# Kernel tuning notes

Measured on AMD Instinct MI355X. Metric: run time of the kernel, lower is better.

The kernel has to match this reference:

```python
import jax, jax.numpy as jnp
import numpy as np

N_NODES = 100000
N_EDGES = 1600000
IN_DIM, HID_DIM, OUT_DIM = 128, 256, 512
BN_EPS = 1e-5


def setup_inputs() -> dict:
    key = jax.random.key(0)
    ks = jax.random.split(key, 10)
    x = jax.random.normal(ks[0], (N_NODES, IN_DIM), dtype=jnp.float32)
    edge_index = jax.random.randint(ks[1], (2, N_EDGES), 0, N_NODES, dtype=jnp.int64)
    def lin(k, o, i):
        return jax.random.normal(k, (o, i), dtype=jnp.float32) * (1.0 / np.sqrt(i))
    return {
        "x": x,
        "edge_index": edge_index,
        # SAGEConv 1: in_dim -> hidden_dim (lin_l has bias, lin_r has none)
        "W1l": lin(ks[2], HID_DIM, IN_DIM),
        "b1": jnp.zeros((HID_DIM,), dtype=jnp.float32),
        "W1r": lin(ks[3], HID_DIM, IN_DIM),
        # BatchNorm1d(hidden_dim)
        "gamma": jnp.ones((HID_DIM,), dtype=jnp.float32),
        "beta": jnp.zeros((HID_DIM,), dtype=jnp.float32),
        # SAGEConv 2: hidden_dim -> gnn_out_dim
        "W2l": lin(ks[4], OUT_DIM, HID_DIM),
        "b2": jnp.zeros((OUT_DIM,), dtype=jnp.float32),
        "W2r": lin(ks[5], OUT_DIM, HID_DIM),
    }


def _sage_max(h, src, dst, Wl, b, Wr, n_nodes):
    # gather source features, max-aggregate onto destination nodes
    agg = jax.ops.segment_max(h[src], dst, num_segments=n_nodes)  # [N, D]
    agg = jnp.where(jnp.isneginf(agg), 0.0, agg)  # PyG fills empty segments with 0
    return agg @ Wl.T + b + h @ Wr.T


def reference(x, edge_index, W1l, b1, W1r, gamma, beta, W2l, b2, W2r):
    src, dst = edge_index[0], edge_index[1]
    n = x.shape[0]
    # layer 1: SAGEConv(in_dim, hidden_dim, aggr='max')
    h = _sage_max(x, src, dst, W1l, b1, W1r, n)
    # BatchNorm1d (batch statistics), Dropout is identity in eval; no activation in 'sage' branch
    mean = jnp.mean(h, axis=0)
    var = jnp.var(h, axis=0)
    h = gamma * (h - mean) * jax.lax.rsqrt(var + BN_EPS) + beta
    # layer 2: SAGEConv(hidden_dim, gnn_out_dim, aggr='max')
    out = _sage_max(h, src, dst, W2l, b2, W2r, n)
    return out
```

## Files before the change

kernel.cpp:

```cpp
#include <hip/hip_runtime.h>
#include <hip/hip_bf16.h>
#include <stdint.h>

#define N_NODES 100000
#define N_EDGES 1600000
#define IN_DIM 128
#define HID_DIM 256
#define OUT_DIM 512
#define NBUK 391
#define BCAP 8192
#define EPB 4096

typedef __attribute__((ext_vector_type(4))) float f32x4;
typedef __attribute__((ext_vector_type(8))) short bf16x8;

__device__ __forceinline__ float bf16lo(uint32_t u){ uint32_t b = u << 16; return __builtin_bit_cast(float, b); }
__device__ __forceinline__ float bf16hi(uint32_t u){ uint32_t b = u & 0xffff0000u; return __builtin_bit_cast(float, b); }
__device__ __forceinline__ uint16_t f32_to_bf16(float f){
  uint32_t u = __builtin_bit_cast(uint32_t, f);
  uint32_t r = (u + 0x7fffu + ((u >> 16) & 1u)) >> 16;
  return (uint16_t)r;
}
__device__ __forceinline__ uint32_t pack_bf16_exact(float lo, float hi){
  return (__builtin_bit_cast(uint32_t, hi) & 0xffff0000u) | (__builtin_bit_cast(uint32_t, lo) >> 16);
}
__device__ __forceinline__ uint32_t pack_bf16_rne(float lo, float hi){
  return (uint32_t)f32_to_bf16(lo) | ((uint32_t)f32_to_bf16(hi) << 16);
}
__device__ __forceinline__ void gl2lds16(const void* g, void* l){
  __builtin_amdgcn_global_load_lds(
      (const __attribute__((address_space(1))) uint32_t*)g,
      (__attribute__((address_space(3))) uint32_t*)l, 16, 0, 0);
}

__global__ void k_convx(const float* __restrict__ x, uint16_t* __restrict__ A1,
                        int* __restrict__ gcur, float* __restrict__ sum,
                        float* __restrict__ sumsq){
  if (blockIdx.x == 12500){
    const int t = threadIdx.x;
    for (int i = t; i < NBUK; i += 256) gcur[i] = i << 13;
    sum[t] = 0.f; sumsq[t] = 0.f;
    return;
  }
  const int idx = blockIdx.x * 256 + threadIdx.x;
  const int n = idx >> 5, q = idx & 31;
  const float4 v = *(const float4*)(x + (long)n * 128 + q * 4);
  ushort4 o;
  o.x = f32_to_bf16(v.x); o.y = f32_to_bf16(v.y);
  o.z = f32_to_bf16(v.z); o.w = f32_to_bf16(v.w);
  *(ushort4*)(A1 + (long)n * 256 + 128 + q * 4) = o;
}

__global__ void k_bucket(const int* __restrict__ src, const int* __restrict__ dst,
                         int* __restrict__ gcur, int* __restrict__ ebuk){
  __shared__ int hist[NBUK], curs[NBUK], base[NBUK];
  const int tid = threadIdx.x;
  const int e0 = blockIdx.x * EPB;
  for (int t = tid; t < NBUK; t += 256) hist[t] = 0;
  __syncthreads();
  for (int i = 0; i < EPB; i += 256){
    int e = e0 + i + tid;
    if (e < N_EDGES) atomicAdd(&hist[dst[e] >> 8], 1);
  }
  __syncthreads();
  for (int t = tid; t < NBUK; t += 256){
    int h = hist[t];
    base[t] = h ? atomicAdd(&gcur[t], h) : 0;
    curs[t] = 0;
  }
  __syncthreads();
  for (int i = 0; i < EPB; i += 256){
    int e = e0 + i + tid;
    if (e < N_EDGES){
      int d = dst[e];
      int b = d >> 8;
      int idx = atomicAdd(&curs[b], 1);
      int pos = base[b] + idx;
      if (pos < ((b + 1) << 13))
        ebuk[pos] = ((d & 255) << 17) | src[e];
    }
  }
}

__global__ __launch_bounds__(256)
void k_fillc(const int* __restrict__ gcur, const int* __restrict__ ebuk,
             int* __restrict__ row_start, int* __restrict__ esrc){
  __shared__ int ebuf[BCAP];
  __shared__ int cnt[256];
  __shared__ int wtot[4];
  __shared__ int red[4];
  const int b = blockIdx.x, tid = threadIdx.x, lane = tid & 63, wv = tid >> 6;
  const int nodebase = b << 8;
  const int nodecnt = min(256, N_NODES - nodebase);
  int accb = 0;
  for (int t = tid; t < b; t += 256) accb += gcur[t] - (t << 13);
  #pragma unroll
  for (int d = 32; d > 0; d >>= 1) accb += __shfl_xor(accb, d);
  if (lane == 0) red[wv] = accb;
  int size_b = gcur[b] - (b << 13);
  if (size_b > BCAP) size_b = BCAP;
  cnt[tid] = 0;
  for (int i = tid; i < size_b; i += 256) ebuf[i] = ebuk[(b << 13) + i];
  __syncthreads();
  const int bs = red[0] + red[1] + red[2] + red[3];
  for (int i = tid; i < size_b; i += 256) atomicAdd(&cnt[ebuf[i] >> 17], 1);
  __syncthreads();
  const int c = cnt[tid];
  int v = c;
  #pragma unroll
  for (int d = 1; d < 64; d <<= 1){ int t = __shfl_up(v, d); if (lane >= d) v += t; }
  if (lane == 63) wtot[wv] = v;
  __syncthreads();
  if (tid < 4){
    int t = wtot[tid];
    #pragma unroll
    for (int d = 1; d < 4; d <<= 1){ int u = __shfl_up(t, d); if (tid >= d) t += u; }
    wtot[tid] = t;
  }
  __syncthreads();
  const int excl = (wv ? wtot[wv - 1] : 0) + (v - c);
  if (tid < nodecnt) row_start[nodebase + tid] = bs + excl;
  if (b == NBUK - 1 && tid == 0) row_start[N_NODES] = N_EDGES;
  cnt[tid] = excl;
  __syncthreads();
  for (int i = tid; i < size_b; i += 256){
    int p = ebuf[i];
    int pos = atomicAdd(&cnt[p >> 17], 1);
    esrc[bs + pos] = p & 0x1FFFF;
  }
}

__global__ void k_w1(const float* __restrict__ W1l, const float* __restrict__ W1r,
                     uint16_t* __restrict__ W1cat){
  int idx = blockIdx.x * 256 + threadIdx.x;
  int j = idx >> 8, k = idx & 255;
  float v = (k < 128) ? W1l[j * 128 + k] : W1r[j * 128 + (k - 128)];
  W1cat[idx] = f32_to_bf16(v);
}

__global__ void k_w2(const float* __restrict__ W2l, const float* __restrict__ W2r,
                     const float* __restrict__ b2, const float* __restrict__ sum,
                     const float* __restrict__ sumsq, const float* __restrict__ gamma,
                     const float* __restrict__ beta, uint16_t* __restrict__ W2cat,
                     float* __restrict__ bias2, float* __restrict__ scale_g,
                     float* __restrict__ shift_g){
  __shared__ float sc_s[256], sh_s[256];
  const int tid = threadIdx.x;
  {
    const float inv_n = 1.0f / (float)N_NODES;
    float mean = sum[tid] * inv_n;
    float var = sumsq[tid] * inv_n - mean * mean;
    float sc = gamma[tid] * rsqrtf(var + 1e-5f);
    float sh = beta[tid] - mean * sc;
    sc_s[tid] = sc; sh_s[tid] = sh;
    if (blockIdx.x == 0){ scale_g[tid] = sc; shift_g[tid] = sh; }
  }
  __syncthreads();
  const int wid = (blockIdx.x * 256 + tid) >> 6;
  const int lane = tid & 63;
  float part = 0.f;
  #pragma unroll
  for (int t = 0; t < 4; t++){
    int k = t * 64 + lane;
    float wl = W2l[(long)wid * 256 + k];
    W2cat[(long)wid * 512 + k] = f32_to_bf16(wl);
    float wr = W2r[(long)wid * 256 + k];
    W2cat[(long)wid * 512 + 256 + k] = f32_to_bf16(wr * sc_s[k]);
    part += sh_s[k] * wr;
  }
  #pragma unroll
  for (int d = 32; d > 0; d >>= 1) part += __shfl_xor(part, d);
  if (lane == 0) bias2[wid] = b2[wid] + part;
}

__global__ void k_agg1(const uint32_t* __restrict__ A1u, const int* __restrict__ row_start,
                       const int* __restrict__ esrc, uint32_t* __restrict__ A1w){
  const int wid = (blockIdx.x * 256 + threadIdx.x) >> 6;
  const int lane = threadIdx.x & 63;
  if (wid >= N_NODES) return;
  const int grp = lane >> 4, li = lane & 15;
  const int s0 = row_start[wid], s1 = row_start[wid + 1];
  float m[8];
  #pragma unroll
  for (int j = 0; j < 8; j++) m[j] = -INFINITY;

  #define ACC1(u)                                        \
    m[0] = fmaxf(m[0], bf16lo(u.x)); m[1] = fmaxf(m[1], bf16hi(u.x)); \
    m[2] = fmaxf(m[2], bf16lo(u.y)); m[3] = fmaxf(m[3], bf16hi(u.y)); \
    m[4] = fmaxf(m[4], bf16lo(u.z)); m[5] = fmaxf(m[5], bf16hi(u.z)); \
    m[6] = fmaxf(m[6], bf16lo(u.w)); m[7] = fmaxf(m[7], bf16hi(u.w));

  int e = s0 + grp;
  for (; e + 12 < s1; e += 16){
    const uint4 ua = *(const uint4*)(A1u + (long)esrc[e] * 128 + 64 + li * 4);
    const uint4 ub = *(const uint4*)(A1u + (long)esrc[e + 4] * 128 + 64 + li * 4);
    const uint4 uc = *(const uint4*)(A1u + (long)esrc[e + 8] * 128 + 64 + li * 4);
    const uint4 ud = *(const uint4*)(A1u + (long)esrc[e + 12] * 128 + 64 + li * 4);
    ACC1(ua); ACC1(ub); ACC1(uc); ACC1(ud);
  }
  for (; e < s1; e += 4){
    const uint4 u = *(const uint4*)(A1u + (long)esrc[e] * 128 + 64 + li * 4);
    ACC1(u);
  }
  #undef ACC1
  #pragma unroll
  for (int j = 0; j < 8; j++){
    m[j] = fmaxf(m[j], __shfl_xor(m[j], 16));
    m[j] = fmaxf(m[j], __shfl_xor(m[j], 32));
  }
  if (grp == 0){
    uint4 o;
    if (s1 == s0){ o.x = o.y = o.z = o.w = 0u; }
    else {
      o.x = pack_bf16_exact(m[0], m[1]);
      o.y = pack_bf16_exact(m[2], m[3]);
      o.z = pack_bf16_exact(m[4], m[5]);
      o.w = pack_bf16_exact(m[6], m[7]);
    }
    *(uint4*)(A1w + (long)wid * 128 + li * 4) = o;
  }
}

__global__ void k_agg2(const uint32_t* __restrict__ A2u, const int* __restrict__ row_start,
                       const int* __restrict__ esrc, const float* __restrict__ scale,
                       const float* __restrict__ shift, uint32_t* __restrict__ A2w){
  const int wid = (blockIdx.x * 256 + threadIdx.x) >> 6;
  const int lane = threadIdx.x & 63;
  if (wid >= N_NODES) return;
  const int half = lane >> 5, li = lane & 31;
  const int c0 = li * 8;
  const float4 sca = *(const float4*)(scale + c0);
  const float4 scb = *(const float4*)(scale + c0 + 4);
  const float4 sha = *(const float4*)(shift + c0);
  const float4 shb = *(const float4*)(shift + c0 + 4);
  const int s0 = row_start[wid], s1 = row_start[wid + 1];
  float m[8];
  #pragma unroll
  for (int j = 0; j < 8; j++) m[j] = -INFINITY;

  #define ACC8(u)                                                   \
    m[0] = fmaxf(m[0], fmaf(bf16lo(u.x), sca.x, sha.x));            \
    m[1] = fmaxf(m[1], fmaf(bf16hi(u.x), sca.y, sha.y));            \
    m[2] = fmaxf(m[2], fmaf(bf16lo(u.y), sca.z, sha.z));            \
    m[3] = fmaxf(m[3], fmaf(bf16hi(u.y), sca.w, sha.w));            \
    m[4] = fmaxf(m[4], fmaf(bf16lo(u.z), scb.x, shb.x));            \
    m[5] = fmaxf(m[5], fmaf(bf16hi(u.z), scb.y, shb.y));            \
    m[6] = fmaxf(m[6], fmaf(bf16lo(u.w), scb.z, shb.z));            \
    m[7] = fmaxf(m[7], fmaf(bf16hi(u.w), scb.w, shb.w));

  int e = s0 + half;
  for (; e + 6 < s1; e += 8){
    const uint4 ua = *(const uint4*)(A2u + (long)esrc[e] * 256 + 128 + li * 4);
    const uint4 ub = *(const uint4*)(A2u + (long)esrc[e + 2] * 256 + 128 + li * 4);
    const uint4 uc = *(const uint4*)(A2u + (long)esrc[e + 4] * 256 + 128 + li * 4);
    const uint4 ud = *(const uint4*)(A2u + (long)esrc[e + 6] * 256 + 128 + li * 4);
    ACC8(ua); ACC8(ub); ACC8(uc); ACC8(ud);
  }
  for (; e < s1; e += 2){
    const uint4 u = *(const uint4*)(A2u + (long)esrc[e] * 256 + 128 + li * 4);
    ACC8(u);
  }
  #undef ACC8
  #pragma unroll
  for (int j = 0; j < 8; j++) m[j] = fmaxf(m[j], __shfl_xor(m[j], 32));
  if (half == 0){
    uint4 o;
    if (s1 == s0){ o.x = 0u; o.y = 0u; o.z = 0u; o.w = 0u; }
    else {
      o.x = pack_bf16_rne(m[0], m[1]);
      o.y = pack_bf16_rne(m[2], m[3]);
      o.z = pack_bf16_rne(m[4], m[5]);
      o.w = pack_bf16_rne(m[6], m[7]);
    }
    *(uint4*)(A2w + (long)wid * 256 + li * 4) = o;
  }
}

template<int KT, bool EPI1>
__global__ __launch_bounds__(256, 2)
void k_gemm(const uint16_t* __restrict__ A, const uint16_t* __restrict__ B,
            const float* __restrict__ bias,
            uint16_t* __restrict__ outb, float* __restrict__ outf,
            float* __restrict__ sum, float* __restrict__ sumsq)
{
  constexpr int KB = KT * 2;
  constexpr int NSTEPS = KT / 64;
  __shared__ uint8_t lds[2][32768];
  const int tid = threadIdx.x, lane = tid & 63, wv = tid >> 6;
  const int wvm = wv >> 1, wvn = wv & 1;
  const int mblk = blockIdx.x, nblk = blockIdx.y;

  f32x4 acc[4][4] = {};

  const int srow = wv * 32 + (lane >> 3);
  const int skb  = (lane & 7) * 16;

  const uint8_t* asrc[4];
  const uint8_t* bsrc[4];
  int kbsw_[4];
  #pragma unroll
  for (int i = 0; i < 4; i++){
    int row = srow + i * 8;
    kbsw_[i] = skb ^ ((row & 7) << 4);
    long grow = (long)mblk * 128 + row;
    if (grow > N_NODES - 1) grow = N_NODES - 1;
    asrc[i] = (const uint8_t*)A + grow * KB + kbsw_[i];
    bsrc[i] = (const uint8_t*)B + ((long)nblk * 128 + row) * KB + kbsw_[i];
  }

  #define STAGE(ks, buf)                                              \
    _Pragma("unroll")                                                 \
    for (int i = 0; i < 4; i++)                                       \
      gl2lds16(asrc[i] + (ks) * 128, &lds[buf][(wv * 4 + i) * 1024]); \
    _Pragma("unroll")                                                 \
    for (int i = 0; i < 4; i++)                                       \
      gl2lds16(bsrc[i] + (ks) * 128, &lds[buf][16384 + (wv * 4 + i) * 1024]);

  STAGE(0, 0);

  #pragma unroll
  for (int ks = 0; ks < NSTEPS; ++ks){
    const int cur = ks & 1;
    if (ks + 1 < NSTEPS){
      STAGE(ks + 1, cur ^ 1);
      asm volatile("s_waitcnt vmcnt(8)" ::: "memory");
    } else {
      asm volatile("s_waitcnt vmcnt(0)" ::: "memory");
    }
    __builtin_amdgcn_s_barrier();
    asm volatile("" ::: "memory");

    const uint8_t* ldsA = &lds[cur][0];
    const uint8_t* ldsB = &lds[cur][16384];
    bf16x8 af[4][2], bfr[4][2];
    #pragma unroll
    for (int m = 0; m < 4; m++){
      int row = wvm * 64 + m * 16 + (lane & 15);
      #pragma unroll
      for (int kk = 0; kk < 2; kk++){
        int kb = kk * 64 + (lane >> 4) * 16;
        af[m][kk] = *(const bf16x8*)(ldsA + row * 128 + (kb ^ ((row & 7) << 4)));
      }
    }
    #pragma unroll
    for (int n = 0; n < 4; n++){
      int row = wvn * 64 + n * 16 + (lane & 15);
      #pragma unroll
      for (int kk = 0; kk < 2; kk++){
        int kb = kk * 64 + (lane >> 4) * 16;
        bfr[n][kk] = *(const bf16x8*)(ldsB + row * 128 + (kb ^ ((row & 7) << 4)));
      }
    }
    #pragma unroll
    for (int kk = 0; kk < 2; kk++)
      #pragma unroll
      for (int m = 0; m < 4; m++)
        #pragma unroll
        for (int n = 0; n < 4; n++)
          acc[m][n] = __builtin_amdgcn_mfma_f32_16x16x32_bf16(af[m][kk], bfr[n][kk], acc[m][n], 0, 0, 0);

    asm volatile("" ::: "memory");
    __builtin_amdgcn_s_barrier();
    asm volatile("" ::: "memory");
  }
  #undef STAGE

  const int rgrp = (lane >> 4) * 4;
  #pragma unroll
  for (int n = 0; n < 4; n++){
    const int col = nblk * 128 + wvn * 64 + n * 16 + (lane & 15);
    const float bv = bias[col];
    float s1v = 0.f, s2v = 0.f;
    #pragma unroll
    for (int m = 0; m < 4; m++){
      const int rowb = mblk * 128 + wvm * 64 + m * 16 + rgrp;
      f32x4 v = acc[m][n];
      #pragma unroll
      for (int j = 0; j < 4; j++){
        const int row = rowb + j;
        const float h = v[j] + bv;
        if (row < N_NODES){
          if (EPI1){
            outb[(long)row * 512 + 256 + col] = f32_to_bf16(h);
            s1v += h; s2v += h * h;
          } else {
            __builtin_nontemporal_store(h, &outf[(long)row * 512 + col]);
          }
        }
      }
    }
    if (EPI1){
      s1v += __shfl_xor(s1v, 16); s1v += __shfl_xor(s1v, 32);
      s2v += __shfl_xor(s2v, 16); s2v += __shfl_xor(s2v, 32);
      if (lane < 16){
        atomicAdd(&sum[col], s1v);
        atomicAdd(&sumsq[col], s2v);
      }
    }
  }
}

extern "C" void kernel_launch(void* const* d_in, const int* in_sizes, int n_in,
                              void* d_out, int out_size, void* d_ws, size_t ws_size,
                              hipStream_t stream){
  const float* x     = (const float*)d_in[0];
  const int*   ei    = (const int*)d_in[1];
  const float* W1l   = (const float*)d_in[2];
  const float* b1    = (const float*)d_in[3];
  const float* W1r   = (const float*)d_in[4];
  const float* gamma = (const float*)d_in[5];
  const float* beta  = (const float*)d_in[6];
  const float* W2l   = (const float*)d_in[7];
  const float* b2    = (const float*)d_in[8];
  const float* W2r   = (const float*)d_in[9];
  const int* esrc_in = ei;
  const int* edst_in = ei + N_EDGES;

  uint8_t* ws = (uint8_t*)d_ws;
  uint16_t* A1       = (uint16_t*)(ws + 0);
  uint16_t* A2       = (uint16_t*)(ws + 51200000);
  int* ebuk          = (int*)(ws + 51200000);
  int* esrc          = (int*)(ws + 153600000);
  int* row_start     = (int*)(ws + 160000000);
  int* gcur          = (int*)(ws + 160402176);
  uint16_t* W1cat    = (uint16_t*)(ws + 160800256);
  uint16_t* W2cat    = (uint16_t*)(ws + 160931328);
  float* bias2       = (float*)(ws + 161455616);
  float* sum         = (float*)(ws + 161457664);
  float* sumsq       = (float*)(ws + 161458688);
  float* scale       = (float*)(ws + 161459712);
  float* shift       = (float*)(ws + 161460736);

  hipLaunchKernelGGL(k_convx, dim3(12501), dim3(256), 0, stream, x, A1, gcur, sum, sumsq);
  hipLaunchKernelGGL(k_bucket, dim3((N_EDGES + EPB - 1) / EPB), dim3(256), 0, stream,
                     esrc_in, edst_in, gcur, ebuk);
  hipLaunchKernelGGL(k_fillc, dim3(NBUK), dim3(256), 0, stream,
                     gcur, ebuk, row_start, esrc);

  hipLaunchKernelGGL(k_w1, dim3(256), dim3(256), 0, stream, W1l, W1r, W1cat);
  hipLaunchKernelGGL(k_agg1, dim3(25000), dim3(256), 0, stream,
                     (const uint32_t*)A1, row_start, esrc, (uint32_t*)A1);

  hipLaunchKernelGGL((k_gemm<256, true>), dim3(782, 2), dim3(256), 0, stream,
                     A1, W1cat, b1, A2, (float*)nullptr, sum, sumsq);

  hipLaunchKernelGGL(k_w2, dim3(128), dim3(256), 0, stream,
                     W2l, W2r, b2, sum, sumsq, gamma, beta, W2cat, bias2, scale, shift);

  hipLaunchKernelGGL(k_agg2, dim3(25000), dim3(256), 0, stream,
                     (const uint32_t*)A2, row_start, esrc, scale, shift, (uint32_t*)A2);

  hipLaunchKernelGGL((k_gemm<512, false>), dim3(782, 4), dim3(256), 0, stream,
                     A2, W2cat, bias2, (uint16_t*)nullptr, (float*)d_out,
                     (float*)nullptr, (float*)nullptr);
}
```

Baseline: 438.3 us.

## Split concatenated activation buffers into separate dense arrays and swap GEMM grid order

The interleaved [agg|self] rows are replaced by separate contiguous buffers for the self features and the aggregated features. The aggregation gathers now read a compact 128- or 256-wide row instead of a strided half of a wider row, which may improve cache-line utilisation for the random gathers. The GEMM takes two A pointers, choosing lo or hi per K-step. The grid is also transposed so the N-blocks sharing one M tile launch next to each other, which should improve L2 reuse of A.

```diff
diff --git a/kernel.cpp b/kernel.cpp
--- a/kernel.cpp
+++ b/kernel.cpp
@@ -33,7 +33,7 @@
       (__attribute__((address_space(3))) uint32_t*)l, 16, 0, 0);
 }
 
-__global__ void k_convx(const float* __restrict__ x, uint16_t* __restrict__ A1,
+__global__ void k_convx(const float* __restrict__ x, uint16_t* __restrict__ X1x,
                         int* __restrict__ gcur, float* __restrict__ sum,
                         float* __restrict__ sumsq){
   if (blockIdx.x == 12500){
@@ -48,7 +48,7 @@
   ushort4 o;
   o.x = f32_to_bf16(v.x); o.y = f32_to_bf16(v.y);
   o.z = f32_to_bf16(v.z); o.w = f32_to_bf16(v.w);
-  *(ushort4*)(A1 + (long)n * 256 + 128 + q * 4) = o;
+  *(ushort4*)(X1x + (long)n * 128 + q * 4) = o;
 }
 
 __global__ void k_bucket(const int* __restrict__ src, const int* __restrict__ dst,
@@ -173,8 +173,8 @@
   if (lane == 0) bias2[wid] = b2[wid] + part;
 }
 
-__global__ void k_agg1(const uint32_t* __restrict__ A1u, const int* __restrict__ row_start,
-                       const int* __restrict__ esrc, uint32_t* __restrict__ A1w){
+__global__ void k_agg1(const uint32_t* __restrict__ X1x, const int* __restrict__ row_start,
+                       const int* __restrict__ esrc, uint32_t* __restrict__ X1agg){
   const int wid = (blockIdx.x * 256 + threadIdx.x) >> 6;
   const int lane = threadIdx.x & 63;
   if (wid >= N_NODES) return;
@@ -192,14 +192,14 @@
 
   int e = s0 + grp;
   for (; e + 12 < s1; e += 16){
-    const uint4 ua = *(const uint4*)(A1u + (long)esrc[e] * 128 + 64 + li * 4);
-    const uint4 ub = *(const uint4*)(A1u + (long)esrc[e + 4] * 128 + 64 + li * 4);
-    const uint4 uc = *(const uint4*)(A1u + (long)esrc[e + 8] * 128 + 64 + li * 4);
-    const uint4 ud = *(const uint4*)(A1u + (long)esrc[e + 12] * 128 + 64 + li * 4);
+    const uint4 ua = *(const uint4*)(X1x + (long)esrc[e] * 64 + li * 4);
+    const uint4 ub = *(const uint4*)(X1x + (long)esrc[e + 4] * 64 + li * 4);
+    const uint4 uc = *(const uint4*)(X1x + (long)esrc[e + 8] * 64 + li * 4);
+    const uint4 ud = *(const uint4*)(X1x + (long)esrc[e + 12] * 64 + li * 4);
     ACC1(ua); ACC1(ub); ACC1(uc); ACC1(ud);
   }
   for (; e < s1; e += 4){
-    const uint4 u = *(const uint4*)(A1u + (long)esrc[e] * 128 + 64 + li * 4);
+    const uint4 u = *(const uint4*)(X1x + (long)esrc[e] * 64 + li * 4);
     ACC1(u);
   }
   #undef ACC1
@@ -217,13 +217,13 @@
       o.z = pack_bf16_exact(m[4], m[5]);
       o.w = pack_bf16_exact(m[6], m[7]);
     }
-    *(uint4*)(A1w + (long)wid * 128 + li * 4) = o;
-  }
-}
-
-__global__ void k_agg2(const uint32_t* __restrict__ A2u, const int* __restrict__ row_start,
+    *(uint4*)(X1agg + (long)wid * 64 + li * 4) = o;
+  }
+}
+
+__global__ void k_agg2(const uint32_t* __restrict__ X2h, const int* __restrict__ row_start,
                        const int* __restrict__ esrc, const float* __restrict__ scale,
-                       const float* __restrict__ shift, uint32_t* __restrict__ A2w){
+                       const float* __restrict__ shift, uint32_t* __restrict__ X2agg){
   const int wid = (blockIdx.x * 256 + threadIdx.x) >> 6;
   const int lane = threadIdx.x & 63;
   if (wid >= N_NODES) return;
@@ -250,14 +250,14 @@
 
   int e = s0 + half;
   for (; e + 6 < s1; e += 8){
-    const uint4 ua = *(const uint4*)(A2u + (long)esrc[e] * 256 + 128 + li * 4);
-    const uint4 ub = *(const uint4*)(A2u + (long)esrc[e + 2] * 256 + 128 + li * 4);
-    const uint4 uc = *(const uint4*)(A2u + (long)esrc[e + 4] * 256 + 128 + li * 4);
-    const uint4 ud = *(const uint4*)(A2u + (long)esrc[e + 6] * 256 + 128 + li * 4);
+    const uint4 ua = *(const uint4*)(X2h + (long)esrc[e] * 128 + li * 4);
+    const uint4 ub = *(const uint4*)(X2h + (long)esrc[e + 2] * 128 + li * 4);
+    const uint4 uc = *(const uint4*)(X2h + (long)esrc[e + 4] * 128 + li * 4);
+    const uint4 ud = *(const uint4*)(X2h + (long)esrc[e + 6] * 128 + li * 4);
     ACC8(ua); ACC8(ub); ACC8(uc); ACC8(ud);
   }
   for (; e < s1; e += 2){
-    const uint4 u = *(const uint4*)(A2u + (long)esrc[e] * 256 + 128 + li * 4);
+    const uint4 u = *(const uint4*)(X2h + (long)esrc[e] * 128 + li * 4);
     ACC8(u);
   }
   #undef ACC8
@@ -272,48 +272,52 @@
       o.z = pack_bf16_rne(m[4], m[5]);
       o.w = pack_bf16_rne(m[6], m[7]);
     }
-    *(uint4*)(A2w + (long)wid * 256 + li * 4) = o;
+    *(uint4*)(X2agg + (long)wid * 128 + li * 4) = o;
   }
 }
 
 template<int KT, bool EPI1>
 __global__ __launch_bounds__(256, 2)
-void k_gemm(const uint16_t* __restrict__ A, const uint16_t* __restrict__ B,
-            const float* __restrict__ bias,
+void k_gemm(const uint16_t* __restrict__ Alo, const uint16_t* __restrict__ Ahi,
+            const uint16_t* __restrict__ B, const float* __restrict__ bias,
             uint16_t* __restrict__ outb, float* __restrict__ outf,
             float* __restrict__ sum, float* __restrict__ sumsq)
 {
-  constexpr int KB = KT * 2;
   constexpr int NSTEPS = KT / 64;
+  constexpr int HSTEPS = NSTEPS / 2;
+  constexpr int NT = EPI1 ? 256 : 512;
   __shared__ uint8_t lds[2][32768];
   const int tid = threadIdx.x, lane = tid & 63, wv = tid >> 6;
   const int wvm = wv >> 1, wvn = wv & 1;
-  const int mblk = blockIdx.x, nblk = blockIdx.y;
+  const int nblk = blockIdx.x, mblk = blockIdx.y;
 
   f32x4 acc[4][4] = {};
 
   const int srow = wv * 32 + (lane >> 3);
   const int skb  = (lane & 7) * 16;
 
-  const uint8_t* asrc[4];
+  const uint8_t* asrc_lo[4];
+  const uint8_t* asrc_hi[4];
   const uint8_t* bsrc[4];
-  int kbsw_[4];
   #pragma unroll
   for (int i = 0; i < 4; i++){
     int row = srow + i * 8;
-    kbsw_[i] = skb ^ ((row & 7) << 4);
+    int kbsw = skb ^ ((row & 7) << 4);
     long grow = (long)mblk * 128 + row;
     if (grow > N_NODES - 1) grow = N_NODES - 1;
-    asrc[i] = (const uint8_t*)A + grow * KB + kbsw_[i];
-    bsrc[i] = (const uint8_t*)B + ((long)nblk * 128 + row) * KB + kbsw_[i];
-  }
-
-  #define STAGE(ks, buf)                                              \
-    _Pragma("unroll")                                                 \
-    for (int i = 0; i < 4; i++)                                       \
-      gl2lds16(asrc[i] + (ks) * 128, &lds[buf][(wv * 4 + i) * 1024]); \
-    _Pragma("unroll")                                                 \
-    for (int i = 0; i < 4; i++)                                       \
+    asrc_lo[i] = (const uint8_t*)Alo + grow * KT + kbsw;
+    asrc_hi[i] = (const uint8_t*)Ahi + grow * KT + kbsw;
+    bsrc[i] = (const uint8_t*)B + ((long)nblk * 128 + row) * (KT * 2) + kbsw;
+  }
+
+  #define STAGE(ks, buf)                                                     \
+    _Pragma("unroll")                                                        \
+    for (int i = 0; i < 4; i++)                                              \
+      gl2lds16((ks) < HSTEPS ? asrc_lo[i] + (ks) * 128                       \
+                             : asrc_hi[i] + ((ks) - HSTEPS) * 128,           \
+               &lds[buf][(wv * 4 + i) * 1024]);                              \
+    _Pragma("unroll")                                                        \
+    for (int i = 0; i < 4; i++)                                              \
       gl2lds16(bsrc[i] + (ks) * 128, &lds[buf][16384 + (wv * 4 + i) * 1024]);
 
   STAGE(0, 0);
@@ -381,10 +385,10 @@
         const float h = v[j] + bv;
         if (row < N_NODES){
           if (EPI1){
-            outb[(long)row * 512 + 256 + col] = f32_to_bf16(h);
+            outb[(long)row * NT + col] = f32_to_bf16(h);
             s1v += h; s2v += h * h;
           } else {
-            __builtin_nontemporal_store(h, &outf[(long)row * 512 + col]);
+            __builtin_nontemporal_store(h, &outf[(long)row * NT + col]);
           }
         }
       }
@@ -417,8 +421,10 @@
   const int* edst_in = ei + N_EDGES;
 
   uint8_t* ws = (uint8_t*)d_ws;
-  uint16_t* A1       = (uint16_t*)(ws + 0);
-  uint16_t* A2       = (uint16_t*)(ws + 51200000);
+  uint16_t* X1agg    = (uint16_t*)(ws + 0);
+  uint16_t* X1x      = (uint16_t*)(ws + 25600000);
+  uint16_t* X2agg    = (uint16_t*)(ws + 51200000);
+  uint16_t* X2h      = (uint16_t*)(ws + 102400000);
   int* ebuk          = (int*)(ws + 51200000);
   int* esrc          = (int*)(ws + 153600000);
   int* row_start     = (int*)(ws + 160000000);
@@ -431,7 +437,7 @@
   float* scale       = (float*)(ws + 161459712);
   float* shift       = (float*)(ws + 161460736);
 
-  hipLaunchKernelGGL(k_convx, dim3(12501), dim3(256), 0, stream, x, A1, gcur, sum, sumsq);
+  hipLaunchKernelGGL(k_convx, dim3(12501), dim3(256), 0, stream, x, X1x, gcur, sum, sumsq);
   hipLaunchKernelGGL(k_bucket, dim3((N_EDGES + EPB - 1) / EPB), dim3(256), 0, stream,
                      esrc_in, edst_in, gcur, ebuk);
   hipLaunchKernelGGL(k_fillc, dim3(NBUK), dim3(256), 0, stream,
@@ -439,18 +445,18 @@
 
   hipLaunchKernelGGL(k_w1, dim3(256), dim3(256), 0, stream, W1l, W1r, W1cat);
   hipLaunchKernelGGL(k_agg1, dim3(25000), dim3(256), 0, stream,
-                     (const uint32_t*)A1, row_start, esrc, (uint32_t*)A1);
-
-  hipLaunchKernelGGL((k_gemm<256, true>), dim3(782, 2), dim3(256), 0, stream,
-                     A1, W1cat, b1, A2, (float*)nullptr, sum, sumsq);
+                     (const uint32_t*)X1x, row_start, esrc, (uint32_t*)X1agg);
+
+  hipLaunchKernelGGL((k_gemm<256, true>), dim3(2, 782), dim3(256), 0, stream,
+                     X1agg, X1x, W1cat, b1, X2h, (float*)nullptr, sum, sumsq);
 
   hipLaunchKernelGGL(k_w2, dim3(128), dim3(256), 0, stream,
                      W2l, W2r, b2, sum, sumsq, gamma, beta, W2cat, bias2, scale, shift);
 
   hipLaunchKernelGGL(k_agg2, dim3(25000), dim3(256), 0, stream,
-                     (const uint32_t*)A2, row_start, esrc, scale, shift, (uint32_t*)A2);
-
-  hipLaunchKernelGGL((k_gemm<512, false>), dim3(782, 4), dim3(256), 0, stream,
-                     A2, W2cat, bias2, (uint16_t*)nullptr, (float*)d_out,
+                     (const uint32_t*)X2h, row_start, esrc, scale, shift, (uint32_t*)X2agg);
+
+  hipLaunchKernelGGL((k_gemm<512, false>), dim3(4, 782), dim3(256), 0, stream,
+                     X2agg, X2h, W2cat, bias2, (uint16_t*)nullptr, (float*)d_out,
                      (float*)nullptr, (float*)nullptr);
 }
```

Result: faster. 412.9 us (-5.8%).
